# Kernel tuning notes

Hardware: AMD Instinct MI355X
Metric: run time of the kernel (lower is better)

## Reference

```python
import jax, jax.numpy as jnp
import numpy as np
from jax import lax

# dims: B batch, C=d_model=256, IMG=128, P=4 patch, H=W=32, L=H*W=1024
# D=d_inner=512 (ssm_ratio 2.0), N=d_state=16, R=dt_rank=16, K=4 scan directions
B, C, IMG, P = 2, 256, 128, 4
H = W = IMG // P
L = H * W
D_INNER, N, R, K = 512, 16, 16, 4


def layernorm(x, g, b, eps=1e-5):
    mu = jnp.mean(x, axis=-1, keepdims=True)
    var = jnp.var(x, axis=-1, keepdims=True)
    return (x - mu) * lax.rsqrt(var + eps) * g + b


def setup_inputs() -> dict:
    key = jax.random.key(0)
    ks = jax.random.split(key, 12)
    f = lambda i, shape, s=0.02: jax.random.normal(ks[i], shape, jnp.float32) * s
    A_init = jnp.tile(jnp.arange(1, N + 1, dtype=jnp.float32)[None, None, :], (K, D_INNER, 1))
    return {
        "x": jax.random.normal(ks[0], (B, C, IMG, IMG), jnp.float32),
        "patch_w": f(1, (C, C, P, P)),
        "patch_b": jnp.zeros((C,), jnp.float32),
        "ln_g": jnp.ones((C,), jnp.float32),
        "ln_b": jnp.zeros((C,), jnp.float32),
        "in_w": f(2, (2 * D_INNER, C)),
        "conv_w": f(3, (D_INNER, 1, 3, 3)),
        "conv_b": jnp.zeros((D_INNER,), jnp.float32),
        "xproj_w": f(4, (K, R + 2 * N, D_INNER)),
        "dt_w": f(5, (K, D_INNER, R)),
        "dt_b": f(6, (K, D_INNER), 0.1),
        "A_log": jnp.log(A_init),
        "Ds": jnp.ones((K, D_INNER), jnp.float32),
        "on_g": jnp.ones((D_INNER,), jnp.float32),
        "on_b": jnp.zeros((D_INNER,), jnp.float32),
        "out_w": f(7, (C, D_INNER)),
        "head_w": f(8, (1, C)),
        "head_b": jnp.zeros((1,), jnp.float32),
    }


def _forward(x, patch_w, patch_b, ln_g, ln_b, in_w, conv_w, conv_b, xproj_w,
             dt_w, dt_b, A_log, Ds, on_g, on_b, out_w, head_w, head_b):
    dn = ("NCHW", "OIHW", "NCHW")
    # GRL is identity in forward. Patch embed conv, stride = patch.
    t = lax.conv_general_dilated(x, patch_w, (P, P), "VALID", dimension_numbers=dn)
    t = t + patch_b[None, :, None, None]
    t = jnp.transpose(t, (0, 2, 3, 1))                      # (B,H,W,C)

    # ---- VSS block: t + SS2D(LN(t)) ----
    u = layernorm(t, ln_g, ln_b)
    xz = jnp.einsum("bhwc,ec->bhwe", u, in_w)               # (B,H,W,2D)
    xc, z = jnp.split(xz, 2, axis=-1)
    xc = jnp.transpose(xc, (0, 3, 1, 2))                    # (B,D,H,W)
    xc = lax.conv_general_dilated(xc, conv_w, (1, 1), "SAME",
                                  dimension_numbers=dn, feature_group_count=D_INNER)
    xc = jax.nn.silu(xc + conv_b[None, :, None, None])

    # cross-scan: row-major, col-major, and their reverses -> (B,K,D,L)
    x_hw = xc.reshape(B, D_INNER, L)
    x_wh = jnp.transpose(xc, (0, 1, 3, 2)).reshape(B, D_INNER, L)
    xs = jnp.stack([x_hw, x_wh], axis=1)
    xs = jnp.concatenate([xs, jnp.flip(xs, axis=-1)], axis=1)  # (B,4,D,L)

    x_dbl = jnp.einsum("bkdl,kcd->bkcl", xs, xproj_w)          # (B,K,R+2N,L)
    dts_r = x_dbl[:, :, :R]
    Bs = x_dbl[:, :, R:R + N]                                  # (B,K,N,L)
    Cs = x_dbl[:, :, R + N:]                                   # (B,K,N,L)
    dts = jnp.einsum("bkrl,kdr->bkdl", dts_r, dt_w) + dt_b[None, :, :, None]
    dts = jax.nn.softplus(dts)                                 # (B,K,D,L)

    A = -jnp.exp(A_log)                                        # (K,D,N)
    dA = jnp.exp(dts[:, :, :, None, :] * A[None, :, :, :, None])      # (B,K,D,N,L)
    dBu = (dts * xs)[:, :, :, None, :] * Bs[:, :, None, :, :]         # (B,K,D,N,L)

    dA_t = jnp.moveaxis(dA, -1, 0)        # (L,B,K,D,N)
    dBu_t = jnp.moveaxis(dBu, -1, 0)
    Cs_t = jnp.moveaxis(Cs, -1, 0)        # (L,B,K,N)

    def step(h, inputs):
        dA_i, dBu_i, C_i = inputs
        h = dA_i * h + dBu_i
        y = jnp.einsum("bkdn,bkn->bkd", h, C_i)
        return h, y

    h0 = jnp.zeros((B, K, D_INNER, N), xs.dtype)
    _, ys = lax.scan(step, h0, (dA_t, dBu_t, Cs_t))           # ys: (L,B,K,D)
    ys = jnp.moveaxis(ys, 0, -1)                               # (B,K,D,L)
    ys = ys + Ds[None, :, :, None] * xs

    # cross-merge (invert the 4 scan orders and sum)
    y_rev = jnp.flip(ys[:, 2:], axis=-1)                        # (B,2,D,L)
    y_hw = ys[:, 0] + y_rev[:, 0]
    y_wh = ys[:, 1] + y_rev[:, 1]
    y_wh = jnp.transpose(y_wh.reshape(B, D_INNER, W, H), (0, 1, 3, 2)).reshape(B, D_INNER, L)
    y = (y_hw + y_wh).reshape(B, D_INNER, H, W)
    y = jnp.transpose(y, (0, 2, 3, 1))                          # (B,H,W,D)

    y = layernorm(y, on_g, on_b) * jax.nn.silu(z)
    ss_out = jnp.einsum("bhwd,cd->bhwc", y, out_w)
    t = t + ss_out

    # global average pool + head
    pooled = jnp.mean(t, axis=(1, 2))                           # (B,C)
    return pooled @ head_w.T + head_b


def reference(x, patch_w, patch_b, ln_g, ln_b, in_w, conv_w, conv_b, xproj_w,
              dt_w, dt_b, A_log, Ds, on_g, on_b, out_w, head_w, head_b):
    return _forward(x, patch_w, patch_b, ln_g, ln_b, in_w, conv_w, conv_b, xproj_w,
                    dt_w, dt_b, A_log, Ds, on_g, on_b, out_w, head_w, head_b)
```

## Files before the change

kernel.cpp:

```cpp
#include <hip/hip_runtime.h>
#include <math.h>


typedef __attribute__((ext_vector_type(4))) float f32x4;
typedef __attribute__((ext_vector_type(8))) short bf16x8;

__device__ __forceinline__ ushort bf16_rn(float f) {
  uint u = __float_as_uint(f);
  return (ushort)((u + 0x7fffu + ((u >> 16) & 1u)) >> 16);
}
__device__ __forceinline__ float bf2f(uint us) { return __uint_as_float(us << 16); }
__device__ __forceinline__ uint packbf(float a, float b) {
  return (uint)bf16_rn(a) | ((uint)bf16_rn(b) << 16);
}

__global__ __launch_bounds__(256) void prep_kernel(const float* __restrict__ x,
    ushort* __restrict__ Ap,
    const float* __restrict__ pw, const float* __restrict__ iw,
    const float* __restrict__ ow, const float* __restrict__ xw,
    ushort* __restrict__ pwh, ushort* __restrict__ pwl,
    ushort* __restrict__ iwh, ushort* __restrict__ iwl,
    ushort* __restrict__ owh, ushort* __restrict__ owl,
    ushort* __restrict__ xwh, ushort* __restrict__ xwl) {
  int bid = blockIdx.x;
  int tid = threadIdx.x;
  if (bid < 2048) {
    __shared__ __align__(16) ushort tile[32][136];
    int b = bid >> 10, hh = (bid >> 5) & 31, c0 = (bid & 31) * 8;
    int ci = tid >> 5, ph = (tid >> 3) & 3, w4 = tid & 7;
    const float* src = x + (((long)(b * 256 + c0 + ci) * 128 + 4 * hh + ph) * 128 + 16 * w4);
    #pragma unroll
    for (int j = 0; j < 4; ++j) {
      float4 v = *(const float4*)(src + 4 * j);
      uint2 pk;
      pk.x = packbf(v.x, v.y);
      pk.y = packbf(v.z, v.w);
      *(uint2*)&tile[w4 * 4 + j][ci * 16 + ph * 4] = pk;
    }
    __syncthreads();
    int w = tid >> 3;
    long rowbase = ((long)(b * 1024 + hh * 32 + w)) * 4096 + c0 * 16;
    #pragma unroll
    for (int i = 0; i < 2; ++i) {
      int gr = (tid & 7) + 8 * i;
      *(uint4*)&Ap[rowbase + gr * 8] = *(const uint4*)&tile[w][gr * 8];
    }
  } else {
    int i = (bid - 2048) * 256 + tid;
    const float* src; ushort* hi; ushort* lo; int off;
    if (i < 1048576)      { src = pw; hi = pwh; lo = pwl; off = i; }
    else if (i < 1310720) { src = iw; hi = iwh; lo = iwl; off = i - 1048576; }
    else if (i < 1441792) { src = ow; hi = owh; lo = owl; off = i - 1310720; }
    else if (i < 1540096) { src = xw; hi = xwh; lo = xwl; off = i - 1441792; }
    else return;
    float f = src[off];
    ushort h = bf16_rn(f);
    hi[off] = h;
    lo[off] = bf16_rn(f - __uint_as_float(((uint)h) << 16));
  }
}

__global__ __launch_bounds__(512) void mfma_bf(
    const ushort* __restrict__ A, const ushort* __restrict__ Bhi,
    const ushort* __restrict__ Blo, float* __restrict__ Cout, float* __restrict__ C2,
    int M, int N, int K, int kchunk, int mode, int NBM, int NBZ)
{
  __shared__ __align__(16) ushort Ah[128 * 64];
  __shared__ __align__(16) ushort Bh[64 * 64];
  __shared__ __align__(16) ushort Bl[64 * 64];
  int tid = threadIdx.x;
  int bid = blockIdx.x;
  int kz = bid % NBZ;
  int n0 = (bid / (NBZ * NBM)) * 64;
  int m0 = ((bid / NBZ) % NBM) * 128;
  int k0 = kz * kchunk;
  int wid = tid >> 6, lane = tid & 63;
  int wm = wid >> 1, wn = wid & 1;
  int lrow = lane & 15, g = lane >> 4;
  f32x4 acc[2][2] = {};
  int nkt = kchunk >> 6;
  for (int kt = 0; kt < nkt; ++kt) {
    int kb = k0 + (kt << 6);
    {
      int gi = tid & 7;
      #pragma unroll
      for (int i = 0; i < 2; ++i) {
        int row = (tid >> 3) + (i << 6);
        uint4 v = *(const uint4*)&A[(long)(m0 + row) * K + kb + gi * 8];
        *(uint4*)&Ah[row * 64 + ((gi ^ (row & 7)) << 3)] = v;
      }
      int row = tid >> 3;
      long off = (long)(n0 + row) * K + kb + gi * 8;
      int la = row * 64 + ((gi ^ (row & 7)) << 3);
      *(uint4*)&Bh[la] = *(const uint4*)&Bhi[off];
      *(uint4*)&Bl[la] = *(const uint4*)&Blo[off];
    }
    __syncthreads();
    #pragma unroll
    for (int kk = 0; kk < 2; ++kk) {
      bf16x8 af[2], bhf[2], blf[2];
      #pragma unroll
      for (int mi = 0; mi < 2; ++mi) {
        int row = wm * 32 + mi * 16 + lrow;
        af[mi] = *(const bf16x8*)&Ah[row * 64 + ((((kk << 2) + g) ^ (row & 7)) << 3)];
      }
      #pragma unroll
      for (int ni = 0; ni < 2; ++ni) {
        int row = wn * 32 + ni * 16 + lrow;
        int col = (((kk << 2) + g) ^ (row & 7)) << 3;
        bhf[ni] = *(const bf16x8*)&Bh[row * 64 + col];
        blf[ni] = *(const bf16x8*)&Bl[row * 64 + col];
      }
      #pragma unroll
      for (int mi = 0; mi < 2; ++mi)
        #pragma unroll
        for (int ni = 0; ni < 2; ++ni) {
          acc[mi][ni] = __builtin_amdgcn_mfma_f32_16x16x32_bf16(af[mi], bhf[ni], acc[mi][ni], 0, 0, 0);
          acc[mi][ni] = __builtin_amdgcn_mfma_f32_16x16x32_bf16(af[mi], blf[ni], acc[mi][ni], 0, 0, 0);
        }
    }
    __syncthreads();
  }
  int r4 = lane >> 4;
  if (mode == 2) {
    bool xhalf = (n0 < 512);
    ushort* xcb = (ushort*)Cout;
    #pragma unroll
    for (int mi = 0; mi < 2; ++mi)
      #pragma unroll
      for (int ni = 0; ni < 2; ++ni) {
        int n = n0 + wn * 32 + ni * 16 + lrow;
        int mb = m0 + wm * 32 + mi * 16 + r4 * 4;
        int bb = mb >> 10, l = mb & 1023;
        if (xhalf) {
          uint2 o;
          o.x = packbf(acc[mi][ni][0], acc[mi][ni][1]);
          o.y = packbf(acc[mi][ni][2], acc[mi][ni][3]);
          *(uint2*)&xcb[((long)(bb * 512 + n)) * 1024 + l] = o;
        } else {
          #pragma unroll
          for (int r = 0; r < 4; ++r)
            C2[(long)(mb + r) * 512 + (n - 512)] = acc[mi][ni][r];
        }
      }
  } else {
    long zoff = (long)kz * M * N;
    #pragma unroll
    for (int mi = 0; mi < 2; ++mi)
      #pragma unroll
      for (int ni = 0; ni < 2; ++ni) {
        int n = n0 + wn * 32 + ni * 16 + lrow;
        int mb = m0 + wm * 32 + mi * 16 + r4 * 4;
        #pragma unroll
        for (int r = 0; r < 4; ++r)
          Cout[zoff + (long)(mb + r) * N + n] = acc[mi][ni][r];
      }
  }
}

__global__ __launch_bounds__(256) void mfma_x(
    const ushort* __restrict__ A, const ushort* __restrict__ Bhi,
    const ushort* __restrict__ Blo, float* __restrict__ xdbl)
{
  __shared__ __align__(16) ushort Ah[64 * 64];
  __shared__ __align__(16) ushort Bh[48 * 64];
  __shared__ __align__(16) ushort Bl[48 * 64];
  int tid = threadIdx.x;
  int m0 = blockIdx.x * 64;
  int z = blockIdx.y, k = z & 3;
  const ushort* Az = A + (long)z * 524288;
  const ushort* Bhz = Bhi + (long)k * 24576;
  const ushort* Blz = Blo + (long)k * 24576;
  int lane = tid & 63, wv = tid >> 6;
  int lrow = lane & 15, g = lane >> 4;
  f32x4 acc[3] = {};
  for (int kt = 0; kt < 8; ++kt) {
    int kb = kt << 6;
    #pragma unroll
    for (int i = 0; i < 2; ++i) {
      int idx = i * 256 + tid;
      int row = idx >> 3, gi = idx & 7;
      uint4 v = *(const uint4*)&Az[(long)(m0 + row) * 512 + kb + gi * 8];
      *(uint4*)&Ah[row * 64 + ((gi ^ (row & 7)) << 3)] = v;
      if (idx < 384) {
        long off = (long)row * 512 + kb + gi * 8;
        int la = row * 64 + ((gi ^ (row & 7)) << 3);
        *(uint4*)&Bh[la] = *(const uint4*)&Bhz[off];
        *(uint4*)&Bl[la] = *(const uint4*)&Blz[off];
      }
    }
    __syncthreads();
    #pragma unroll
    for (int kk = 0; kk < 2; ++kk) {
      int arow = wv * 16 + lrow;
      bf16x8 af = *(const bf16x8*)&Ah[arow * 64 + ((((kk << 2) + g) ^ (arow & 7)) << 3)];
      #pragma unroll
      for (int ni = 0; ni < 3; ++ni) {
        int brow = ni * 16 + lrow;
        int col = (((kk << 2) + g) ^ (brow & 7)) << 3;
        bf16x8 bh = *(const bf16x8*)&Bh[brow * 64 + col];
        bf16x8 bl = *(const bf16x8*)&Bl[brow * 64 + col];
        acc[ni] = __builtin_amdgcn_mfma_f32_16x16x32_bf16(af, bh, acc[ni], 0, 0, 0);
        acc[ni] = __builtin_amdgcn_mfma_f32_16x16x32_bf16(af, bl, acc[ni], 0, 0, 0);
      }
    }
    __syncthreads();
  }
  float* Cz = xdbl + (long)z * 49152;
  int r4 = lane >> 4;
  #pragma unroll
  for (int ni = 0; ni < 3; ++ni) {
    int n = ni * 16 + lrow;
    int mb = m0 + wv * 16 + r4 * 4;
    #pragma unroll
    for (int r = 0; r < 4; ++r)
      Cz[(long)(mb + r) * 48 + n] = acc[ni][r];
  }
}

__global__ __launch_bounds__(256) void reduce_split(const float* __restrict__ P,
    float* __restrict__ C, const float* __restrict__ bias,
    int MN, int N, int S, int accumulate) {
  int i = blockIdx.x * 256 + threadIdx.x;
  if (i * 4 >= MN) return;
  float4 v = make_float4(0.f, 0.f, 0.f, 0.f);
  for (int s = 0; s < S; ++s) {
    float4 p = *(const float4*)(P + (long)s * MN + i * 4);
    v.x += p.x; v.y += p.y; v.z += p.z; v.w += p.w;
  }
  if (bias) {
    float4 bv = *(const float4*)(bias + ((i * 4) & (N - 1)));
    v.x += bv.x; v.y += bv.y; v.z += bv.z; v.w += bv.w;
  }
  if (accumulate) {
    float4 o = *(const float4*)(C + (long)i * 4);
    v.x += o.x; v.y += o.y; v.z += o.z; v.w += o.w;
  }
  *(float4*)(C + (long)i * 4) = v;
}

__device__ __forceinline__ float blk_sum(float v, float* sm) {
  #pragma unroll
  for (int o = 32; o > 0; o >>= 1) v += __shfl_down(v, o);
  int wid = threadIdx.x >> 6, lane = threadIdx.x & 63;
  __syncthreads();
  if (lane == 0) sm[wid] = v;
  __syncthreads();
  int nw = blockDim.x >> 6;
  float r = 0.f;
  for (int i = 0; i < nw; ++i) r += sm[i];
  return r;
}

__global__ __launch_bounds__(256) void reduce_ln1(const float* __restrict__ P,
    float* __restrict__ t, const float* __restrict__ bias,
    const float* __restrict__ g, const float* __restrict__ b,
    ushort* __restrict__ u) {
  __shared__ float sm[8];
  int m = blockIdx.x, c = threadIdx.x;
  float v = bias[c];
  #pragma unroll
  for (int s = 0; s < 8; ++s) v += P[(long)s * 524288 + m * 256 + c];
  t[(long)m * 256 + c] = v;
  float s1 = blk_sum(v, sm);
  float s2 = blk_sum(v * v, sm);
  float mu = s1 * (1.f / 256.f);
  float var = s2 * (1.f / 256.f) - mu * mu;
  float rs = rsqrtf(var + 1e-5f);
  u[(long)m * 256 + c] = bf16_rn((v - mu) * rs * g[c] + b[c]);
}

__global__ __launch_bounds__(256) void dwconv_kernel(const ushort* __restrict__ xc,
    const float* __restrict__ cw, const float* __restrict__ cb, ushort* __restrict__ out) {
  __shared__ float plane[32][33];
  int d = blockIdx.x, b = blockIdx.y;
  long base = ((long)b * 512 + d) * 1024;
  int tid = threadIdx.x;
  uint2 v = *(const uint2*)&xc[base + tid * 4];
  int h0 = (tid * 4) >> 5, w0 = (tid * 4) & 31;
  plane[h0][w0 + 0] = bf2f(v.x & 0xffff); plane[h0][w0 + 1] = bf2f(v.x >> 16);
  plane[h0][w0 + 2] = bf2f(v.y & 0xffff); plane[h0][w0 + 3] = bf2f(v.y >> 16);
  float w9[9];
  #pragma unroll
  for (int i = 0; i < 9; ++i) w9[i] = cw[d * 9 + i];
  float bias = cb[d];
  __syncthreads();
  float o4[4];
  #pragma unroll
  for (int j = 0; j < 4; ++j) {
    int p = tid * 4 + j, h = p >> 5, w = p & 31;
    float acc = 0.f;
    #pragma unroll
    for (int dh = -1; dh <= 1; ++dh) {
      int hy = h + dh;
      if (hy < 0 || hy > 31) continue;
      #pragma unroll
      for (int dw = -1; dw <= 1; ++dw) {
        int wx = w + dw;
        if (wx < 0 || wx > 31) continue;
        acc += w9[(dh + 1) * 3 + (dw + 1)] * plane[hy][wx];
      }
    }
    acc += bias;
    o4[j] = acc / (1.f + __expf(-acc));
  }
  uint2 o2;
  o2.x = packbf(o4[0], o4[1]);
  o2.y = packbf(o4[2], o4[3]);
  *(uint2*)&out[base + tid * 4] = o2;
}

__global__ __launch_bounds__(256) void build_xsT(const ushort* __restrict__ xca,
    ushort* __restrict__ xsTb) {
  __shared__ ushort tile[32][34];
  int h = blockIdx.x;
  int d0 = blockIdx.y * 32;
  int z = blockIdx.z;
  int b = z >> 2, k = z & 3;
  int tid = threadIdx.x;
  int a = tid >> 5, q = tid & 31;
  #pragma unroll
  for (int i = 0; i < 4; ++i) {
    int di = a + i * 8;
    tile[di][q] = xca[((long)(b * 512 + d0 + di)) * 1024 + h * 32 + q];
  }
  __syncthreads();
  #pragma unroll
  for (int i = 0; i < 4; ++i) {
    int w = a + i * 8;
    int r;
    if (k == 0) r = h * 32 + w;
    else if (k == 1) r = w * 32 + h;
    else if (k == 2) r = 1023 - (h * 32 + w);
    else r = 1023 - (w * 32 + h);
    xsTb[((long)z * 1024 + r) * 512 + d0 + q] = tile[q][w];
  }
}

template<bool FINAL>
__global__ __launch_bounds__(128) void scan_chunk6(
    const float* __restrict__ xdbl, ushort* xsb,
    const float* __restrict__ dtw, const float* __restrict__ dtb,
    const float* __restrict__ A_log, const float* __restrict__ Ds,
    float* __restrict__ dsum, float* __restrict__ hpb)
{
  __shared__ float sdt[32][64];
  __shared__ float sxv[16][64];
  __shared__ float sy[16][64];
  __shared__ float sBC[32][32];
  float (*sR)[16] = (float(*)[16])sy;
  int tid = threadIdx.x;
  int dl = tid >> 1, ng = tid & 1;
  int d0 = blockIdx.x * 64;
  int d = d0 + dl;
  int c = blockIdx.y;
  int z = blockIdx.z;
  int k = z & 3;
  long baseD = (long)z * 524288;
  int l0 = c * 32;
  const float* xdz = xdbl + (long)z * 49152 + (long)l0 * 48;
  #pragma unroll
  for (int i = 0; i < 2; ++i) {
    int idx = i * 128 + tid;
    int l = idx >> 3, q = idx & 7;
    *(float4*)&sBC[l][q * 4] = *(const float4*)(xdz + l * 48 + 16 + q * 4);
  }
  {
    int l = tid >> 2, q = tid & 3;
    *(float4*)&sR[l][q * 4] = *(const float4*)(xdz + l * 48 + q * 4);
  }
  float a[8], h[8];
  #pragma unroll
  for (int j = 0; j < 8; ++j) {
    a[j] = -__expf(A_log[((long)k * 512 + d) * 16 + ng * 8 + j]);
    h[j] = 0.f;
  }
  float4 wr0 = *(const float4*)(dtw + ((long)k * 512 + d) * 16);
  float4 wr1 = *(const float4*)(dtw + ((long)k * 512 + d) * 16 + 4);
  float4 wr2 = *(const float4*)(dtw + ((long)k * 512 + d) * 16 + 8);
  float4 wr3 = *(const float4*)(dtw + ((long)k * 512 + d) * 16 + 12);
  float dbias = dtb[k * 512 + d];
  int gbase = c * 65536 + z * 8192 + d * 16 + ng * 8;
  float Dv = 0.f;
  if (FINAL) {
    #pragma unroll
    for (int j = 0; j < 8; ++j) h[j] = hpb[gbase + j];
    Dv = Ds[k * 512 + d];
  }
  __syncthreads();
  #pragma unroll
  for (int li = 0; li < 16; ++li) {
    int l = ng * 16 + li;
    const float* rr = &sR[l][0];
    float acc = dbias;
    acc += wr0.x * rr[0];  acc += wr0.y * rr[1];  acc += wr0.z * rr[2];  acc += wr0.w * rr[3];
    acc += wr1.x * rr[4];  acc += wr1.y * rr[5];  acc += wr1.z * rr[6];  acc += wr1.w * rr[7];
    acc += wr2.x * rr[8];  acc += wr2.y * rr[9];  acc += wr2.z * rr[10]; acc += wr2.w * rr[11];
    acc += wr3.x * rr[12]; acc += wr3.y * rr[13]; acc += wr3.z * rr[14]; acc += wr3.w * rr[15];
    sdt[l][dl] = (acc > 20.f) ? acc : __logf(1.f + __expf(acc));
  }
  __syncthreads();
  int xli = tid >> 3;
  int xdj = (tid & 7) * 8;
  uint4 rxv = *(const uint4*)&xsb[baseD + (long)(l0 + xli) * 512 + d0 + xdj];
  float dtsum = 0.f;
  for (int t = 0; t < 2; ++t) {
    {
      float4 f0, f1;
      f0.x = bf2f(rxv.x & 0xffff); f0.y = bf2f(rxv.x >> 16);
      f0.z = bf2f(rxv.y & 0xffff); f0.w = bf2f(rxv.y >> 16);
      f1.x = bf2f(rxv.z & 0xffff); f1.y = bf2f(rxv.z >> 16);
      f1.z = bf2f(rxv.w & 0xffff); f1.w = bf2f(rxv.w >> 16);
      *(float4*)&sxv[xli][xdj] = f0;
      *(float4*)&sxv[xli][xdj + 4] = f1;
    }
    __syncthreads();
    if (t == 0)
      rxv = *(const uint4*)&xsb[baseD + (long)(l0 + 16 + xli) * 512 + d0 + xdj];
    #pragma unroll
    for (int li = 0; li < 16; ++li) {
      int lr = t * 16 + li;
      float dt = sdt[lr][dl];
      float xv = sxv[li][dl];
      float w = dt * xv;
      float4 B0 = *(const float4*)&sBC[lr][ng * 8];
      float4 B1 = *(const float4*)&sBC[lr][ng * 8 + 4];
      if (!FINAL) {
        dtsum += dt;
        h[0] = __expf(dt * a[0]) * h[0] + w * B0.x;
        h[1] = __expf(dt * a[1]) * h[1] + w * B0.y;
        h[2] = __expf(dt * a[2]) * h[2] + w * B0.z;
        h[3] = __expf(dt * a[3]) * h[3] + w * B0.w;
        h[4] = __expf(dt * a[4]) * h[4] + w * B1.x;
        h[5] = __expf(dt * a[5]) * h[5] + w * B1.y;
        h[6] = __expf(dt * a[6]) * h[6] + w * B1.z;
        h[7] = __expf(dt * a[7]) * h[7] + w * B1.w;
      } else {
        float4 C0 = *(const float4*)&sBC[lr][16 + ng * 8];
        float4 C1 = *(const float4*)&sBC[lr][16 + ng * 8 + 4];
        float p;
        h[0] = __expf(dt * a[0]) * h[0] + w * B0.x; p  = h[0] * C0.x;
        h[1] = __expf(dt * a[1]) * h[1] + w * B0.y; p += h[1] * C0.y;
        h[2] = __expf(dt * a[2]) * h[2] + w * B0.z; p += h[2] * C0.z;
        h[3] = __expf(dt * a[3]) * h[3] + w * B0.w; p += h[3] * C0.w;
        h[4] = __expf(dt * a[4]) * h[4] + w * B1.x; p += h[4] * C1.x;
        h[5] = __expf(dt * a[5]) * h[5] + w * B1.y; p += h[5] * C1.y;
        h[6] = __expf(dt * a[6]) * h[6] + w * B1.z; p += h[6] * C1.z;
        h[7] = __expf(dt * a[7]) * h[7] + w * B1.w; p += h[7] * C1.w;
        p += __shfl_xor(p, 1);
        if (ng == 0) sy[li][dl] = p + Dv * xv;
      }
    }
    __syncthreads();
    if (FINAL) {
      float4 f0 = *(float4*)&sy[xli][xdj];
      float4 f1 = *(float4*)&sy[xli][xdj + 4];
      uint4 o;
      o.x = packbf(f0.x, f0.y); o.y = packbf(f0.z, f0.w);
      o.z = packbf(f1.x, f1.y); o.w = packbf(f1.z, f1.w);
      *(uint4*)&xsb[baseD + (long)(l0 + t * 16 + xli) * 512 + d0 + xdj] = o;
    }
  }
  if (!FINAL) {
    *(float4*)(hpb + gbase)     = make_float4(h[0], h[1], h[2], h[3]);
    *(float4*)(hpb + gbase + 4) = make_float4(h[4], h[5], h[6], h[7]);
    if (ng == 0) dsum[c * 4096 + z * 512 + d] = dtsum;
  }
}

__global__ __launch_bounds__(256) void scan_prefix(const float* __restrict__ dsum,
    const float* __restrict__ A_log, float* __restrict__ hpb) {
  int g = blockIdx.x * 256 + threadIdx.x;
  int z = g >> 13, n = g & 15;
  int d = (g >> 4) & 511;
  int k = z & 3;
  float a = -__expf(A_log[((long)k * 512 + d) * 16 + n]);
  float h = 0.f;
  #pragma unroll
  for (int c = 0; c < 32; ++c) {
    float P = __expf(dsum[c * 4096 + z * 512 + d] * a);
    float hp = hpb[c * 65536 + g];
    hpb[c * 65536 + g] = h;
    h = P * h + hp;
  }
}

__global__ __launch_bounds__(256) void combine_ln2gate(const ushort* __restrict__ ys,
    const float* __restrict__ zb, ushort* __restrict__ out,
    const float* __restrict__ g, const float* __restrict__ b) {
  __shared__ float sm[8];
  int m = blockIdx.x, tid = threadIdx.x;
  int bb = m >> 10, l = m & 1023;
  int hh = l >> 5, w = l & 31;
  int lw = w * 32 + hh;
  long b4 = (long)bb * 4;
  uint u0 = *(const uint*)&ys[((b4 + 0) * 1024 + l) * 512 + tid * 2];
  uint u1 = *(const uint*)&ys[((b4 + 2) * 1024 + (1023 - l)) * 512 + tid * 2];
  uint u2 = *(const uint*)&ys[((b4 + 1) * 1024 + lw) * 512 + tid * 2];
  uint u3 = *(const uint*)&ys[((b4 + 3) * 1024 + (1023 - lw)) * 512 + tid * 2];
  float v0 = bf2f(u0 & 0xffff) + bf2f(u1 & 0xffff) + bf2f(u2 & 0xffff) + bf2f(u3 & 0xffff);
  float v1 = bf2f(u0 >> 16) + bf2f(u1 >> 16) + bf2f(u2 >> 16) + bf2f(u3 >> 16);
  float s1 = blk_sum(v0 + v1, sm);
  float s2 = blk_sum(v0 * v0 + v1 * v1, sm);
  float mu = s1 * (1.f / 512.f);
  float var = s2 * (1.f / 512.f) - mu * mu;
  float rs = rsqrtf(var + 1e-5f);
  float2 gg = *(const float2*)(g + tid * 2);
  float2 bbv = *(const float2*)(b + tid * 2);
  float2 zz = *(const float2*)(zb + (long)m * 512 + tid * 2);
  float y0 = ((v0 - mu) * rs * gg.x + bbv.x) * (zz.x / (1.f + __expf(-zz.x)));
  float y1 = ((v1 - mu) * rs * gg.y + bbv.y) * (zz.y / (1.f + __expf(-zz.y)));
  *(uint*)&out[(long)m * 512 + tid * 2] = packbf(y0, y1);
}

__global__ __launch_bounds__(256) void head_partial(const float* __restrict__ t,
    const float* __restrict__ hw, float* __restrict__ part) {
  __shared__ float sm[8];
  int j = blockIdx.x, b = blockIdx.y;
  int c = threadIdx.x;
  float s = 0.f;
  for (int l = j * 64; l < j * 64 + 64; ++l) s += t[((long)b * 1024 + l) * 256 + c];
  s *= hw[c];
  float tot = blk_sum(s, sm);
  if (c == 0) part[b * 16 + j] = tot;
}

__global__ void head_final(const float* __restrict__ part, const float* __restrict__ hb, float* __restrict__ out) {
  int tid = threadIdx.x;
  float v = (tid < 32) ? part[tid] : 0.f;
  #pragma unroll
  for (int o = 1; o < 16; o <<= 1) v += __shfl_xor(v, o);
  if (tid < 32 && (tid & 15) == 0) out[tid >> 4] = v * (1.f / 1024.f) + hb[0];
}

extern "C" void kernel_launch(void* const* d_in, const int* in_sizes, int n_in,
                              void* d_out, int out_size, void* d_ws, size_t ws_size,
                              hipStream_t stream) {
  const float* x       = (const float*)d_in[0];
  const float* patch_w = (const float*)d_in[1];
  const float* patch_b = (const float*)d_in[2];
  const float* ln_g    = (const float*)d_in[3];
  const float* ln_b    = (const float*)d_in[4];
  const float* in_w    = (const float*)d_in[5];
  const float* conv_w  = (const float*)d_in[6];
  const float* conv_b  = (const float*)d_in[7];
  const float* xproj_w = (const float*)d_in[8];
  const float* dt_w    = (const float*)d_in[9];
  const float* dt_b    = (const float*)d_in[10];
  const float* A_log   = (const float*)d_in[11];
  const float* Ds      = (const float*)d_in[12];
  const float* on_g    = (const float*)d_in[13];
  const float* on_b    = (const float*)d_in[14];
  const float* out_w   = (const float*)d_in[15];
  const float* head_w  = (const float*)d_in[16];
  const float* head_b  = (const float*)d_in[17];

  float* ws = (float*)d_ws;
  float* t_buf   = ws;
  float* u_buf   = t_buf + 524288;
  float* xz_buf  = u_buf + 524288;
  float* xc_buf  = xz_buf + 2097152;
  float* xca_buf = xc_buf + 1048576;
  float* xsT_buf = xca_buf + 1048576;
  float* xdbl_buf= xsT_buf + 4194304;
  float* spl_buf = xdbl_buf + 393216;
  float* part_buf= spl_buf + 4194304;
  float* tail    = part_buf + 32;
  ushort* A_p    = (ushort*)xsT_buf;
  ushort* pw_hi  = (ushort*)xz_buf;
  ushort* pw_lo  = (ushort*)(xz_buf + 524288);
  float*  z_buf  = xz_buf;
  float*  P_patch= spl_buf;
  float*  P_out  = spl_buf;
  ushort* u_bf   = (ushort*)u_buf;
  ushort* xc_bf  = (ushort*)xc_buf;
  ushort* xca_bf = (ushort*)xca_buf;
  ushort* y_bf   = (ushort*)xca_buf;
  ushort* iw_hi  = (ushort*)tail;
  ushort* iw_lo  = (ushort*)(tail + 131072);
  ushort* ow_hi  = (ushort*)(tail + 262144);
  ushort* ow_lo  = (ushort*)(tail + 327680);
  ushort* xw_hi  = (ushort*)(tail + 393216);
  ushort* xw_lo  = (ushort*)(tail + 442368);
  ushort* xsT_bf = (ushort*)(tail + 491520);
  float*  dsum_buf = tail + 2588672;
  float*  hp_buf   = tail + 2719744;

  prep_kernel<<<8065, 256, 0, stream>>>(x, A_p, patch_w, in_w, out_w, xproj_w,
      pw_hi, pw_lo, iw_hi, iw_lo, ow_hi, ow_lo, xw_hi, xw_lo);
  mfma_bf<<<512, 512, 0, stream>>>(A_p, pw_hi, pw_lo, P_patch, nullptr,
      2048, 256, 4096, 512, 0, 16, 8);
  reduce_ln1<<<2048, 256, 0, stream>>>(P_patch, t_buf, patch_b, ln_g, ln_b, u_bf);
  mfma_bf<<<256, 512, 0, stream>>>(u_bf, iw_hi, iw_lo, xc_buf, z_buf,
      2048, 1024, 256, 256, 2, 16, 1);
  dwconv_kernel<<<dim3(512, 2), 256, 0, stream>>>(xc_bf, conv_w, conv_b, xca_bf);
  build_xsT<<<dim3(32, 16, 8), 256, 0, stream>>>(xca_bf, xsT_bf);
  mfma_x<<<dim3(16, 8), 256, 0, stream>>>(xsT_bf, xw_hi, xw_lo, xdbl_buf);
  scan_chunk6<false><<<dim3(8, 32, 8), 128, 0, stream>>>(xdbl_buf, xsT_bf,
      dt_w, dt_b, A_log, Ds, dsum_buf, hp_buf);
  scan_prefix<<<256, 256, 0, stream>>>(dsum_buf, A_log, hp_buf);
  scan_chunk6<true><<<dim3(8, 32, 8), 128, 0, stream>>>(xdbl_buf, xsT_bf,
      dt_w, dt_b, A_log, Ds, nullptr, hp_buf);
  combine_ln2gate<<<2048, 256, 0, stream>>>(xsT_bf, z_buf, y_bf, on_g, on_b);
  mfma_bf<<<256, 512, 0, stream>>>(y_bf, ow_hi, ow_lo, P_out, nullptr,
      2048, 256, 512, 128, 0, 16, 4);
  reduce_split<<<512, 256, 0, stream>>>(P_out, t_buf, nullptr, 524288, 256, 4, 1);
  head_partial<<<dim3(16, 2), 256, 0, stream>>>(t_buf, head_w, part_buf);
  head_final<<<1, 64, 0, stream>>>(part_buf, head_b, (float*)d_out);
}
```

Before: 133.3 us.

## Drop patch-weight lo split and fold head projection into reductions

The patch-embed GEMM now uses only the bf16 high part of the weights, which halves its B-tile loads and MFMA count, at some cost in precision. Because pooling and the head are linear, the head dot product is also computed per token inside the LN1 reduction and the output-projection split reduction. This removes the writes and reads of the full residual buffer and removes the head_partial kernel. The accuracy risk comes from dropping the lo correction term on a K=4096 reduction.

```diff
diff --git a/kernel.cpp b/kernel.cpp
--- a/kernel.cpp
+++ b/kernel.cpp
@@ -18,7 +18,7 @@
     ushort* __restrict__ Ap,
     const float* __restrict__ pw, const float* __restrict__ iw,
     const float* __restrict__ ow, const float* __restrict__ xw,
-    ushort* __restrict__ pwh, ushort* __restrict__ pwl,
+    ushort* __restrict__ pwh,
     ushort* __restrict__ iwh, ushort* __restrict__ iwl,
     ushort* __restrict__ owh, ushort* __restrict__ owl,
     ushort* __restrict__ xwh, ushort* __restrict__ xwl) {
@@ -47,9 +47,12 @@
     }
   } else {
     int i = (bid - 2048) * 256 + tid;
+    if (i < 1048576) {
+      pwh[i] = bf16_rn(pw[i]);
+      return;
+    }
     const float* src; ushort* hi; ushort* lo; int off;
-    if (i < 1048576)      { src = pw; hi = pwh; lo = pwl; off = i; }
-    else if (i < 1310720) { src = iw; hi = iwh; lo = iwl; off = i - 1048576; }
+    if (i < 1310720)      { src = iw; hi = iwh; lo = iwl; off = i - 1048576; }
     else if (i < 1441792) { src = ow; hi = owh; lo = owl; off = i - 1310720; }
     else if (i < 1540096) { src = xw; hi = xwh; lo = xwl; off = i - 1441792; }
     else return;
@@ -63,7 +66,7 @@
 __global__ __launch_bounds__(512) void mfma_bf(
     const ushort* __restrict__ A, const ushort* __restrict__ Bhi,
     const ushort* __restrict__ Blo, float* __restrict__ Cout, float* __restrict__ C2,
-    int M, int N, int K, int kchunk, int mode, int NBM, int NBZ)
+    int M, int N, int K, int kchunk, int mode, int NBM, int NBZ, int uselo)
 {
   __shared__ __align__(16) ushort Ah[128 * 64];
   __shared__ __align__(16) ushort Bh[64 * 64];
@@ -93,12 +96,12 @@
       long off = (long)(n0 + row) * K + kb + gi * 8;
       int la = row * 64 + ((gi ^ (row & 7)) << 3);
       *(uint4*)&Bh[la] = *(const uint4*)&Bhi[off];
-      *(uint4*)&Bl[la] = *(const uint4*)&Blo[off];
+      if (uselo) *(uint4*)&Bl[la] = *(const uint4*)&Blo[off];
     }
     __syncthreads();
     #pragma unroll
     for (int kk = 0; kk < 2; ++kk) {
-      bf16x8 af[2], bhf[2], blf[2];
+      bf16x8 af[2], bhf[2];
       #pragma unroll
       for (int mi = 0; mi < 2; ++mi) {
         int row = wm * 32 + mi * 16 + lrow;
@@ -109,15 +112,23 @@
         int row = wn * 32 + ni * 16 + lrow;
         int col = (((kk << 2) + g) ^ (row & 7)) << 3;
         bhf[ni] = *(const bf16x8*)&Bh[row * 64 + col];
-        blf[ni] = *(const bf16x8*)&Bl[row * 64 + col];
       }
       #pragma unroll
       for (int mi = 0; mi < 2; ++mi)
         #pragma unroll
+        for (int ni = 0; ni < 2; ++ni)
+          acc[mi][ni] = __builtin_amdgcn_mfma_f32_16x16x32_bf16(af[mi], bhf[ni], acc[mi][ni], 0, 0, 0);
+      if (uselo) {
+        #pragma unroll
         for (int ni = 0; ni < 2; ++ni) {
-          acc[mi][ni] = __builtin_amdgcn_mfma_f32_16x16x32_bf16(af[mi], bhf[ni], acc[mi][ni], 0, 0, 0);
-          acc[mi][ni] = __builtin_amdgcn_mfma_f32_16x16x32_bf16(af[mi], blf[ni], acc[mi][ni], 0, 0, 0);
+          int row = wn * 32 + ni * 16 + lrow;
+          int col = (((kk << 2) + g) ^ (row & 7)) << 3;
+          bf16x8 blf = *(const bf16x8*)&Bl[row * 64 + col];
+          #pragma unroll
+          for (int mi = 0; mi < 2; ++mi)
+            acc[mi][ni] = __builtin_amdgcn_mfma_f32_16x16x32_bf16(af[mi], blf, acc[mi][ni], 0, 0, 0);
         }
+      }
     }
     __syncthreads();
   }
@@ -218,27 +229,6 @@
   }
 }
 
-__global__ __launch_bounds__(256) void reduce_split(const float* __restrict__ P,
-    float* __restrict__ C, const float* __restrict__ bias,
-    int MN, int N, int S, int accumulate) {
-  int i = blockIdx.x * 256 + threadIdx.x;
-  if (i * 4 >= MN) return;
-  float4 v = make_float4(0.f, 0.f, 0.f, 0.f);
-  for (int s = 0; s < S; ++s) {
-    float4 p = *(const float4*)(P + (long)s * MN + i * 4);
-    v.x += p.x; v.y += p.y; v.z += p.z; v.w += p.w;
-  }
-  if (bias) {
-    float4 bv = *(const float4*)(bias + ((i * 4) & (N - 1)));
-    v.x += bv.x; v.y += bv.y; v.z += bv.z; v.w += bv.w;
-  }
-  if (accumulate) {
-    float4 o = *(const float4*)(C + (long)i * 4);
-    v.x += o.x; v.y += o.y; v.z += o.z; v.w += o.w;
-  }
-  *(float4*)(C + (long)i * 4) = v;
-}
-
 __device__ __forceinline__ float blk_sum(float v, float* sm) {
   #pragma unroll
   for (int o = 32; o > 0; o >>= 1) v += __shfl_down(v, o);
@@ -253,21 +243,52 @@
 }
 
 __global__ __launch_bounds__(256) void reduce_ln1(const float* __restrict__ P,
-    float* __restrict__ t, const float* __restrict__ bias,
-    const float* __restrict__ g, const float* __restrict__ b,
-    ushort* __restrict__ u) {
+    const float* __restrict__ bias, const float* __restrict__ g,
+    const float* __restrict__ b, ushort* __restrict__ u,
+    const float* __restrict__ hw, float* __restrict__ tpart) {
   __shared__ float sm[8];
   int m = blockIdx.x, c = threadIdx.x;
   float v = bias[c];
   #pragma unroll
   for (int s = 0; s < 8; ++s) v += P[(long)s * 524288 + m * 256 + c];
-  t[(long)m * 256 + c] = v;
   float s1 = blk_sum(v, sm);
   float s2 = blk_sum(v * v, sm);
+  float s3 = blk_sum(v * hw[c], sm);
+  if (c == 0) tpart[m] = s3;
   float mu = s1 * (1.f / 256.f);
   float var = s2 * (1.f / 256.f) - mu * mu;
   float rs = rsqrtf(var + 1e-5f);
   u[(long)m * 256 + c] = bf16_rn((v - mu) * rs * g[c] + b[c]);
+}
+
+__global__ __launch_bounds__(256) void reduce_ss(const float* __restrict__ P,
+    const float* __restrict__ hw, float* __restrict__ spart) {
+  __shared__ float sm[8];
+  int bid = blockIdx.x;
+  int i = bid * 1024 + threadIdx.x * 4;
+  float4 v = make_float4(0.f, 0.f, 0.f, 0.f);
+  #pragma unroll
+  for (int s = 0; s < 4; ++s) {
+    float4 p = *(const float4*)(P + (long)s * 524288 + i);
+    v.x += p.x; v.y += p.y; v.z += p.z; v.w += p.w;
+  }
+  float4 w = *(const float4*)(hw + (i & 255));
+  float s = v.x * w.x + v.y * w.y + v.z * w.z + v.w * w.w;
+  float tot = blk_sum(s, sm);
+  if (threadIdx.x == 0) spart[bid] = tot;
+}
+
+__global__ __launch_bounds__(256) void head_final(const float* __restrict__ tpart,
+    const float* __restrict__ spart, const float* __restrict__ hb,
+    float* __restrict__ out) {
+  __shared__ float sm[8];
+  int b = blockIdx.x, tid = threadIdx.x;
+  float s = 0.f;
+  #pragma unroll
+  for (int j = 0; j < 4; ++j) s += tpart[b * 1024 + tid * 4 + j];
+  s += spart[b * 256 + tid];
+  float tot = blk_sum(s, sm);
+  if (tid == 0) out[b] = tot * (1.f / 1024.f) + hb[0];
 }
 
 __global__ __launch_bounds__(256) void dwconv_kernel(const ushort* __restrict__ xc,
@@ -513,26 +534,6 @@
   *(uint*)&out[(long)m * 512 + tid * 2] = packbf(y0, y1);
 }
 
-__global__ __launch_bounds__(256) void head_partial(const float* __restrict__ t,
-    const float* __restrict__ hw, float* __restrict__ part) {
-  __shared__ float sm[8];
-  int j = blockIdx.x, b = blockIdx.y;
-  int c = threadIdx.x;
-  float s = 0.f;
-  for (int l = j * 64; l < j * 64 + 64; ++l) s += t[((long)b * 1024 + l) * 256 + c];
-  s *= hw[c];
-  float tot = blk_sum(s, sm);
-  if (c == 0) part[b * 16 + j] = tot;
-}
-
-__global__ void head_final(const float* __restrict__ part, const float* __restrict__ hb, float* __restrict__ out) {
-  int tid = threadIdx.x;
-  float v = (tid < 32) ? part[tid] : 0.f;
-  #pragma unroll
-  for (int o = 1; o < 16; o <<= 1) v += __shfl_xor(v, o);
-  if (tid < 32 && (tid & 15) == 0) out[tid >> 4] = v * (1.f / 1024.f) + hb[0];
-}
-
 extern "C" void kernel_launch(void* const* d_in, const int* in_sizes, int n_in,
                               void* d_out, int out_size, void* d_ws, size_t ws_size,
                               hipStream_t stream) {
@@ -564,11 +565,11 @@
   float* xsT_buf = xca_buf + 1048576;
   float* xdbl_buf= xsT_buf + 4194304;
   float* spl_buf = xdbl_buf + 393216;
-  float* part_buf= spl_buf + 4194304;
-  float* tail    = part_buf + 32;
+  float* tail    = spl_buf + 4194304;
+  float*  tpart  = t_buf;
+  float*  spart  = t_buf + 2048;
   ushort* A_p    = (ushort*)xsT_buf;
   ushort* pw_hi  = (ushort*)xz_buf;
-  ushort* pw_lo  = (ushort*)(xz_buf + 524288);
   float*  z_buf  = xz_buf;
   float*  P_patch= spl_buf;
   float*  P_out  = spl_buf;
@@ -587,12 +588,13 @@
   float*  hp_buf   = tail + 2719744;
 
   prep_kernel<<<8065, 256, 0, stream>>>(x, A_p, patch_w, in_w, out_w, xproj_w,
-      pw_hi, pw_lo, iw_hi, iw_lo, ow_hi, ow_lo, xw_hi, xw_lo);
-  mfma_bf<<<512, 512, 0, stream>>>(A_p, pw_hi, pw_lo, P_patch, nullptr,
-      2048, 256, 4096, 512, 0, 16, 8);
-  reduce_ln1<<<2048, 256, 0, stream>>>(P_patch, t_buf, patch_b, ln_g, ln_b, u_bf);
+      pw_hi, iw_hi, iw_lo, ow_hi, ow_lo, xw_hi, xw_lo);
+  mfma_bf<<<512, 512, 0, stream>>>(A_p, pw_hi, nullptr, P_patch, nullptr,
+      2048, 256, 4096, 512, 0, 16, 8, 0);
+  reduce_ln1<<<2048, 256, 0, stream>>>(P_patch, patch_b, ln_g, ln_b, u_bf,
+      head_w, tpart);
   mfma_bf<<<256, 512, 0, stream>>>(u_bf, iw_hi, iw_lo, xc_buf, z_buf,
-      2048, 1024, 256, 256, 2, 16, 1);
+      2048, 1024, 256, 256, 2, 16, 1, 1);
   dwconv_kernel<<<dim3(512, 2), 256, 0, stream>>>(xc_bf, conv_w, conv_b, xca_bf);
   build_xsT<<<dim3(32, 16, 8), 256, 0, stream>>>(xca_bf, xsT_bf);
   mfma_x<<<dim3(16, 8), 256, 0, stream>>>(xsT_bf, xw_hi, xw_lo, xdbl_buf);
@@ -603,8 +605,7 @@
       dt_w, dt_b, A_log, Ds, nullptr, hp_buf);
   combine_ln2gate<<<2048, 256, 0, stream>>>(xsT_bf, z_buf, y_bf, on_g, on_b);
   mfma_bf<<<256, 512, 0, stream>>>(y_bf, ow_hi, ow_lo, P_out, nullptr,
-      2048, 256, 512, 128, 0, 16, 4);
-  reduce_split<<<512, 256, 0, stream>>>(P_out, t_buf, nullptr, 524288, 256, 4, 1);
-  head_partial<<<dim3(16, 2), 256, 0, stream>>>(t_buf, head_w, part_buf);
-  head_final<<<1, 64, 0, stream>>>(part_buf, head_b, (float*)d_out);
-}
+      2048, 256, 512, 128, 0, 16, 4, 1);
+  reduce_ss<<<512, 256, 0, stream>>>(P_out, head_w, spart);
+  head_final<<<2, 256, 0, stream>>>(tpart, spart, head_b, (float*)d_out);
+}
```

After: 127.8 us. -4.1%, faster.
